# Performance work log

Measured on AMD Instinct MI355X. Metric: run time of the kernel, lower is better.

## Reference

```python
import jax, jax.numpy as jnp
import numpy as np

N, E, F_IN, F_HID, F_OUT = 100000, 1600000, 128, 128, 64


def setup_inputs() -> dict:
    key = jax.random.key(0)
    k = jax.random.split(key, 6)
    x = jax.random.normal(k[0], (N, F_IN), dtype=jnp.float32)
    edge_index = jax.random.randint(k[1], (2, E), 0, N, dtype=jnp.int32)
    # Glorot-ish init for the two GCNConv linear layers (+ bias, PyG default bias=True)
    W1 = jax.random.normal(k[2], (F_IN, F_HID), dtype=jnp.float32) * (1.0 / np.sqrt(F_IN))
    b1 = jnp.zeros((F_HID,), dtype=jnp.float32)
    W2 = jax.random.normal(k[3], (F_HID, F_OUT), dtype=jnp.float32) * (1.0 / np.sqrt(F_HID))
    b2 = jnp.zeros((F_OUT,), dtype=jnp.float32)
    return {"x": x, "edge_index": edge_index, "W1": W1, "b1": b1, "W2": W2, "b2": b2}


def reference(x, edge_index, W1, b1, W2, b2):
    n = x.shape[0]
    row, col = edge_index[0], edge_index[1]
    # gcn_norm with add_self_loops=True, edge_weight=None -> all-ones weights
    loop = jnp.arange(n, dtype=row.dtype)
    row = jnp.concatenate([row, loop])
    col = jnp.concatenate([col, loop])
    w = jnp.ones(row.shape[0], dtype=x.dtype)
    deg = jax.ops.segment_sum(w, col, num_segments=n)  # in-degree at targets
    dis = jnp.where(deg > 0, jax.lax.rsqrt(jnp.maximum(deg, 1.0)), 0.0)
    norm = dis[row] * w * dis[col]  # [E+N]

    def gcn_conv(h, W, b):
        h = h @ W                       # linear transform first (PyG order)
        msg = h[row] * norm[:, None]    # gather + scale, [E+N, d]
        return jax.ops.segment_sum(msg, col, num_segments=n) + b  # scatter-add

    h = jax.nn.relu(gcn_conv(x, W1, b1))
    # dropout is identity in eval mode
    return gcn_conv(h, W2, b2)
```

## Files before the change

kernel.cpp:

```cpp
#include <hip/hip_runtime.h>

#define F1 128
#define F2 64
#define BSH 9
#define BSZ 512
#define BFILL_CAP 12288

typedef unsigned int u32;
typedef unsigned short u16;
typedef __attribute__((ext_vector_type(8))) short bf16x8;
typedef __attribute__((ext_vector_type(4))) float f32x4;

__device__ __forceinline__ u32 bf16rne(float f) {
    u32 u = __float_as_uint(f);
    return (u + 0x7FFFu + ((u >> 16) & 1u)) >> 16;
}
__device__ __forceinline__ u32 pack2(float lo, float hi) {
    return bf16rne(lo) | (bf16rne(hi) << 16);
}
__device__ __forceinline__ float bflo(u32 u) { return __uint_as_float(u << 16); }
__device__ __forceinline__ float bfhi(u32 u) { return __uint_as_float(u & 0xFFFF0000u); }

__device__ __forceinline__ void acc8(float* ax, uint4 v) {
    ax[0] += bflo(v.x); ax[1] += bfhi(v.x);
    ax[2] += bflo(v.y); ax[3] += bfhi(v.y);
    ax[4] += bflo(v.z); ax[5] += bfhi(v.z);
    ax[6] += bflo(v.w); ax[7] += bfhi(v.w);
}


__global__ __launch_bounds__(256) void k_bhist(const int* __restrict__ colv,
                                               int* __restrict__ bucket_cnt, int E) {
    __shared__ int l[256];
    int t = threadIdx.x;
    l[t] = 0;
    __syncthreads();
    for (int e = blockIdx.x * blockDim.x + t; e < E; e += gridDim.x * blockDim.x)
        atomicAdd(&l[colv[e] >> BSH], 1);
    __syncthreads();
    if (l[t]) atomicAdd(&bucket_cnt[t], l[t]);
}

__global__ __launch_bounds__(256) void k_bscan(const int* __restrict__ bucket_cnt,
                                               int* __restrict__ bucket_base,
                                               int* __restrict__ bucket_cur,
                                               int* __restrict__ rowptr_last,
                                               int NB, int E) {
    __shared__ int s[256];
    int t = threadIdx.x;
    int v = (t < NB) ? bucket_cnt[t] : 0;
    s[t] = v;
    __syncthreads();
    for (int d = 1; d < 256; d <<= 1) {
        int u = (t >= d) ? s[t - d] : 0;
        __syncthreads();
        s[t] += u;
        __syncthreads();
    }
    int excl = s[t] - v;
    if (t < NB) { bucket_base[t] = excl; bucket_cur[t] = excl; }
    if (t == NB - 1) bucket_base[NB] = s[t];
    if (t == 0) *rowptr_last = E;
}

__global__ __launch_bounds__(256) void k_part(const int* __restrict__ rowv,
                                              const int* __restrict__ colv,
                                              int* __restrict__ bucket_cur,
                                              u32* __restrict__ ebuf, int E) {
    __shared__ int lcnt[256], lexcl[256], lcur[256], lbase[256];
    __shared__ int stot;
    __shared__ u32 sval[4096];
    __shared__ u16 sbkt[4096];
    int t = threadIdx.x;
    lcnt[t] = 0;
    __syncthreads();
    int rows[16], cols[16];
    int e0 = blockIdx.x * 4096;
#pragma unroll
    for (int it = 0; it < 16; it++) {
        int e = e0 + it * 256 + t;
        bool v = e < E;
        cols[it] = v ? colv[e] : -1;
        rows[it] = v ? rowv[e] : 0;
        if (v) atomicAdd(&lcnt[cols[it] >> BSH], 1);
    }
    __syncthreads();
    int v = lcnt[t];
    int s = v;
    lexcl[t] = s;
    __syncthreads();
    for (int d = 1; d < 256; d <<= 1) {
        int u = (t >= d) ? lexcl[t - d] : 0;
        __syncthreads();
        lexcl[t] += u;
        __syncthreads();
    }
    int incl = lexcl[t];
    __syncthreads();
    lexcl[t] = incl - v;
    lcur[t] = incl - v;
    if (v) lbase[t] = atomicAdd(&bucket_cur[t], v);
    if (t == 255) stot = incl;
    __syncthreads();
#pragma unroll
    for (int it = 0; it < 16; it++) {
        if (cols[it] >= 0) {
            int b = cols[it] >> BSH;
            int pos = atomicAdd(&lcur[b], 1);
            sval[pos] = ((u32)(cols[it] & (BSZ - 1)) << 17) | (u32)rows[it];
            sbkt[pos] = (u16)b;
        }
    }
    __syncthreads();
    int total = stot;
    for (int i = t; i < total; i += 256) {
        int b = sbkt[i];
        ebuf[lbase[b] + (i - lexcl[b])] = sval[i];
    }
}

__global__ __launch_bounds__(512) void k_bfill(const u32* __restrict__ ebuf,
                                               const int* __restrict__ bucket_base,
                                               int* __restrict__ rowptr,
                                               float* __restrict__ dis,
                                               int* __restrict__ adj, int N) {
    __shared__ int cnt[BSZ], scn[BSZ], cur[BSZ];
    __shared__ int sadj[BFILL_CAP];
    int t = threadIdx.x;
    int b = blockIdx.x;
    int e0 = bucket_base[b], e1 = bucket_base[b + 1];
    int len = e1 - e0;
    cnt[t] = 0;
    __syncthreads();
    for (int i = e0 + t; i < e1; i += BSZ)
        atomicAdd(&cnt[ebuf[i] >> 17], 1);
    __syncthreads();
    scn[t] = cnt[t];
    __syncthreads();
    for (int d = 1; d < BSZ; d <<= 1) {
        int u = (t >= d) ? scn[t - d] : 0;
        __syncthreads();
        scn[t] += u;
        __syncthreads();
    }
    int excl = scn[t] - cnt[t];
    cur[t] = excl;
    int node = (b << BSH) + t;
    if (node < N) {
        rowptr[node] = e0 + excl;
        dis[node] = rsqrtf((float)(cnt[t] + 1));
    }
    __syncthreads();
    if (len <= BFILL_CAP) {
        for (int i = e0 + t; i < e1; i += BSZ) {
            u32 p = ebuf[i];
            int c = p >> 17;
            int r = (int)(p & 0x1FFFFu);
            int pos = atomicAdd(&cur[c], 1);
            sadj[pos] = r;
        }
        __syncthreads();
        for (int i = t; i < len; i += BSZ)
            adj[e0 + i] = sadj[i];
    } else {
        for (int i = e0 + t; i < e1; i += BSZ) {
            u32 p = ebuf[i];
            int c = p >> 17;
            int r = (int)(p & 0x1FFFFu);
            int pos = atomicAdd(&cur[c], 1);
            adj[e0 + pos] = r;
        }
    }
}


__device__ __forceinline__ void wprep_do(const float* __restrict__ W,
                                         uint4* __restrict__ wf, int NBc, int t) {
    int lane = t & 63;
    int rem = t >> 6;
    int nb = rem % NBc;
    int kb = rem / NBc;
    int C = NBc * 16;
    int col = nb * 16 + (lane & 15);
    int krow = kb * 32 + (lane >> 4) * 8;
    u32 w[4];
#pragma unroll
    for (int p = 0; p < 4; p++) {
        float lo = W[(size_t)(krow + 2 * p) * C + col];
        float hi = W[(size_t)(krow + 2 * p + 1) * C + col];
        w[p] = pack2(lo, hi);
    }
    wf[t] = make_uint4(w[0], w[1], w[2], w[3]);
}

__global__ __launch_bounds__(256) void k_wprep(const float* __restrict__ W1,
                                               const float* __restrict__ W2,
                                               uint4* __restrict__ w1f,
                                               uint4* __restrict__ w2f) {
    int blk = blockIdx.x;
    if (blk < 8) wprep_do(W1, w1f, 8, blk * 256 + threadIdx.x);
    else         wprep_do(W2, w2f, 4, (blk - 8) * 256 + threadIdx.x);
}


__global__ __launch_bounds__(256, 4) void k_gemm1(const float* __restrict__ x,
                                                  const uint4* __restrict__ w1f,
                                                  const float* __restrict__ dis,
                                                  u16* __restrict__ gb, int N) {
    int lane = threadIdx.x & 63;
    int wave = threadIdx.x >> 6;
    int m = lane & 15, quad = lane >> 4;
    int row0 = blockIdx.x * 64 + wave * 16;
    int arow = min(row0 + m, N - 1);
    const float* xr = x + (size_t)arow * F1 + quad * 8;
    bf16x8 a[4];
#pragma unroll
    for (int kb = 0; kb < 4; kb++) {
        float4 lo = *(const float4*)(xr + kb * 32);
        float4 hi = *(const float4*)(xr + kb * 32 + 4);
        a[kb][0] = (short)bf16rne(lo.x); a[kb][1] = (short)bf16rne(lo.y);
        a[kb][2] = (short)bf16rne(lo.z); a[kb][3] = (short)bf16rne(lo.w);
        a[kb][4] = (short)bf16rne(hi.x); a[kb][5] = (short)bf16rne(hi.y);
        a[kb][6] = (short)bf16rne(hi.z); a[kb][7] = (short)bf16rne(hi.w);
    }
    f32x4 acc[8];
#pragma unroll
    for (int nb = 0; nb < 8; nb++) acc[nb] = (f32x4)(0.0f);
#pragma unroll
    for (int nb = 0; nb < 8; nb++) {
#pragma unroll
        for (int kb = 0; kb < 4; kb++) {
            uint4 braw = w1f[(kb * 8 + nb) * 64 + lane];
            bf16x8 bf = *(bf16x8*)&braw;
            acc[nb] = __builtin_amdgcn_mfma_f32_16x16x32_bf16(a[kb], bf, acc[nb], 0, 0, 0);
        }
    }
    float dv[4];
    int rbase = row0 + quad * 4;
#pragma unroll
    for (int reg = 0; reg < 4; reg++) dv[reg] = dis[min(rbase + reg, N - 1)];
#pragma unroll
    for (int reg = 0; reg < 4; reg++) {
        int r = rbase + reg;
        if (r < N) {
            u16* gr = gb + (size_t)r * F1 + m;
#pragma unroll
            for (int nb = 0; nb < 8; nb++)
                gr[nb * 16] = (u16)bf16rne(acc[nb][reg] * dv[reg]);
        }
    }
}


__global__ __launch_bounds__(256) void k_agg1(const uint4* __restrict__ g1,
                                              const int* __restrict__ rowptr,
                                              const int* __restrict__ adj,
                                              const float* __restrict__ dis,
                                              const float* __restrict__ b,
                                              uint4* __restrict__ z, int N) {
    int node = __builtin_amdgcn_readfirstlane(blockIdx.x * 4 + (threadIdx.x >> 6));
    if (node >= N) return;
    int lane = threadIdx.x & 63;
    int grp = lane >> 4;
    int sub = lane & 15;
    float ax[8];
#pragma unroll
    for (int i = 0; i < 8; i++) ax[i] = 0.0f;
    int s = rowptr[node], e = rowptr[node + 1];
    if (grp == 0) acc8(ax, g1[(size_t)node * 16 + sub]);
    const uint4 z4 = make_uint4(0u, 0u, 0u, 0u);
    int i0 = s + grp;
    bool p0 = i0 < e, p1 = i0 + 4 < e, p2 = i0 + 8 < e, p3 = i0 + 12 < e;
    int c0 = 0, c1 = 0, c2 = 0, c3 = 0;
    if (p0) c0 = adj[i0];
    if (p1) c1 = adj[i0 + 4];
    if (p2) c2 = adj[i0 + 8];
    if (p3) c3 = adj[i0 + 12];
    for (int j = s; j < e; j += 16) {
        uint4 v0 = z4, v1 = z4, v2 = z4, v3 = z4;
        if (p0) v0 = g1[(size_t)c0 * 16 + sub];
        if (p1) v1 = g1[(size_t)c1 * 16 + sub];
        if (p2) v2 = g1[(size_t)c2 * 16 + sub];
        if (p3) v3 = g1[(size_t)c3 * 16 + sub];
        int in0 = j + 16 + grp;
        p0 = in0 < e; p1 = in0 + 4 < e; p2 = in0 + 8 < e; p3 = in0 + 12 < e;
        if (p0) c0 = adj[in0];
        if (p1) c1 = adj[in0 + 4];
        if (p2) c2 = adj[in0 + 8];
        if (p3) c3 = adj[in0 + 12];
        acc8(ax, v0);
        acc8(ax, v1);
        acc8(ax, v2);
        acc8(ax, v3);
    }
#pragma unroll
    for (int i = 0; i < 8; i++) {
        ax[i] += __shfl_xor(ax[i], 16);
        ax[i] += __shfl_xor(ax[i], 32);
    }
    if (grp == 0) {
        float d = dis[node];
        float4 b0 = *(const float4*)(b + 8 * sub);
        float4 b1 = *(const float4*)(b + 8 * sub + 4);
        float o[8];
        o[0] = fmaxf(fmaf(d, ax[0], b0.x), 0.0f);
        o[1] = fmaxf(fmaf(d, ax[1], b0.y), 0.0f);
        o[2] = fmaxf(fmaf(d, ax[2], b0.z), 0.0f);
        o[3] = fmaxf(fmaf(d, ax[3], b0.w), 0.0f);
        o[4] = fmaxf(fmaf(d, ax[4], b1.x), 0.0f);
        o[5] = fmaxf(fmaf(d, ax[5], b1.y), 0.0f);
        o[6] = fmaxf(fmaf(d, ax[6], b1.z), 0.0f);
        o[7] = fmaxf(fmaf(d, ax[7], b1.w), 0.0f);
        uint4 ov;
        ov.x = pack2(o[0], o[1]); ov.y = pack2(o[2], o[3]);
        ov.z = pack2(o[4], o[5]); ov.w = pack2(o[6], o[7]);
        z[(size_t)node * 16 + sub] = ov;
    }
}


__global__ __launch_bounds__(256, 4) void k_gemm2(const u32* __restrict__ z,
                                                  const uint4* __restrict__ w2f,
                                                  const float* __restrict__ dis,
                                                  u16* __restrict__ gb, int N) {
    int lane = threadIdx.x & 63;
    int wave = threadIdx.x >> 6;
    int m = lane & 15, quad = lane >> 4;
    int row0 = blockIdx.x * 64 + wave * 16;
    int arow = min(row0 + m, N - 1);
    const u32* zr = z + (size_t)arow * 64 + quad * 4;
    bf16x8 a[4];
#pragma unroll
    for (int kb = 0; kb < 4; kb++) {
        uint4 za = *(const uint4*)(zr + kb * 16);
        a[kb] = *(bf16x8*)&za;
    }
    f32x4 acc[4];
#pragma unroll
    for (int nb = 0; nb < 4; nb++) acc[nb] = (f32x4)(0.0f);
#pragma unroll
    for (int nb = 0; nb < 4; nb++) {
#pragma unroll
        for (int kb = 0; kb < 4; kb++) {
            uint4 braw = w2f[(kb * 4 + nb) * 64 + lane];
            bf16x8 bf = *(bf16x8*)&braw;
            acc[nb] = __builtin_amdgcn_mfma_f32_16x16x32_bf16(a[kb], bf, acc[nb], 0, 0, 0);
        }
    }
    float dv[4];
    int rbase = row0 + quad * 4;
#pragma unroll
    for (int reg = 0; reg < 4; reg++) dv[reg] = dis[min(rbase + reg, N - 1)];
#pragma unroll
    for (int reg = 0; reg < 4; reg++) {
        int r = rbase + reg;
        if (r < N) {
            u16* gr = gb + (size_t)r * F2 + m;
#pragma unroll
            for (int nb = 0; nb < 4; nb++)
                gr[nb * 16] = (u16)bf16rne(acc[nb][reg] * dv[reg]);
        }
    }
}


__global__ __launch_bounds__(256) void k_agg2(const uint4* __restrict__ g,
                                              const int* __restrict__ rowptr,
                                              const int* __restrict__ adj,
                                              const float* __restrict__ dis,
                                              const float* __restrict__ b,
                                              float* __restrict__ out, int N) {
    int node = __builtin_amdgcn_readfirstlane(blockIdx.x * 4 + (threadIdx.x >> 6));
    if (node >= N) return;
    int lane = threadIdx.x & 63;
    int grp = lane >> 3;
    int sub = lane & 7;
    float ax[8];
#pragma unroll
    for (int i = 0; i < 8; i++) ax[i] = 0.0f;
    int s = rowptr[node], e = rowptr[node + 1];
    if (grp == 0) acc8(ax, g[(size_t)node * 8 + sub]);
    const uint4 z4 = make_uint4(0u, 0u, 0u, 0u);
    int i0 = s + grp;
    bool p0 = i0 < e, p1 = i0 + 8 < e, p2 = i0 + 16 < e, p3 = i0 + 24 < e;
    int c0 = 0, c1 = 0, c2 = 0, c3 = 0;
    if (p0) c0 = adj[i0];
    if (p1) c1 = adj[i0 + 8];
    if (p2) c2 = adj[i0 + 16];
    if (p3) c3 = adj[i0 + 24];
    for (int j = s; j < e; j += 32) {
        uint4 v0 = z4, v1 = z4, v2 = z4, v3 = z4;
        if (p0) v0 = g[(size_t)c0 * 8 + sub];
        if (p1) v1 = g[(size_t)c1 * 8 + sub];
        if (p2) v2 = g[(size_t)c2 * 8 + sub];
        if (p3) v3 = g[(size_t)c3 * 8 + sub];
        int in0 = j + 32 + grp;
        p0 = in0 < e; p1 = in0 + 8 < e; p2 = in0 + 16 < e; p3 = in0 + 24 < e;
        if (p0) c0 = adj[in0];
        if (p1) c1 = adj[in0 + 8];
        if (p2) c2 = adj[in0 + 16];
        if (p3) c3 = adj[in0 + 24];
        acc8(ax, v0);
        acc8(ax, v1);
        acc8(ax, v2);
        acc8(ax, v3);
    }
#pragma unroll
    for (int i = 0; i < 8; i++) {
        ax[i] += __shfl_xor(ax[i], 8);
        ax[i] += __shfl_xor(ax[i], 16);
        ax[i] += __shfl_xor(ax[i], 32);
    }
    if (grp == 0) {
        float d = dis[node];
        float4 b0 = *(const float4*)(b + 8 * sub);
        float4 b1 = *(const float4*)(b + 8 * sub + 4);
        float4 o0, o1;
        o0.x = fmaf(d, ax[0], b0.x); o0.y = fmaf(d, ax[1], b0.y);
        o0.z = fmaf(d, ax[2], b0.z); o0.w = fmaf(d, ax[3], b0.w);
        o1.x = fmaf(d, ax[4], b1.x); o1.y = fmaf(d, ax[5], b1.y);
        o1.z = fmaf(d, ax[6], b1.z); o1.w = fmaf(d, ax[7], b1.w);
        float4* op = (float4*)(out + (size_t)node * F2 + 8 * sub);
        op[0] = o0;
        op[1] = o1;
    }
}


extern "C" void kernel_launch(void* const* d_in, const int* in_sizes, int n_in,
                              void* d_out, int out_size, void* d_ws, size_t ws_size,
                              hipStream_t stream) {
    const float* x  = (const float*)d_in[0];
    const int*   ei = (const int*)d_in[1];
    const float* W1 = (const float*)d_in[2];
    const float* b1 = (const float*)d_in[3];
    const float* W2 = (const float*)d_in[4];
    const float* b2 = (const float*)d_in[5];
    float* out = (float*)d_out;

    const int N = in_sizes[0] / F1;
    const int E = in_sizes[1] / 2;
    const int NB = (N + BSZ - 1) >> BSH;
    const int* rowv = ei;
    const int* colv = ei + E;

    char* ws = (char*)d_ws;
    size_t off = 0;
    auto take = [&](size_t bytes) -> void* {
        void* p = ws + off;
        off += (bytes + 255) & ~(size_t)255;
        return p;
    };
    u16*   g1b     = (u16*)take((size_t)N * F1 * 2);
    u32*   zb      = (u32*)take((size_t)N * 64 * 4);
    u16*   g2b     = g1b;
    u32*   ebuf    = (u32*)g1b;
    float* dis     = (float*)take((size_t)N * 4);
    int*   rowptr  = (int*)take((size_t)(N + 1) * 4);
    int*   adj     = (int*)take((size_t)E * 4);
    uint4* w1f     = (uint4*)take(4 * 8 * 64 * 16);
    uint4* w2f     = (uint4*)take(4 * 4 * 64 * 16);
    int*   bucket_cnt  = (int*)take(256 * 4);
    int*   bucket_base = (int*)take(257 * 4);
    int*   bucket_cur  = (int*)take(256 * 4);

    hipMemsetAsync(bucket_cnt, 0, 256 * 4, stream);

    k_wprep<<<12, 256, 0, stream>>>(W1, W2, w1f, w2f);

    k_bhist<<<256, 256, 0, stream>>>(colv, bucket_cnt, E);
    k_bscan<<<1, 256, 0, stream>>>(bucket_cnt, bucket_base, bucket_cur, rowptr + N, NB, E);
    k_part<<<(E + 4095) / 4096, 256, 0, stream>>>(rowv, colv, bucket_cur, ebuf, E);
    k_bfill<<<NB, BSZ, 0, stream>>>(ebuf, bucket_base, rowptr, dis, adj, N);

    int gblocks = (N + 63) / 64;
    k_gemm1<<<gblocks, 256, 0, stream>>>(x, w1f, dis, g1b, N);
    k_agg1<<<(N + 3) / 4, 256, 0, stream>>>((const uint4*)g1b, rowptr, adj, dis, b1,
                                            (uint4*)zb, N);
    k_gemm2<<<gblocks, 256, 0, stream>>>(zb, w2f, dis, g2b, N);
    k_agg2<<<(N + 3) / 4, 256, 0, stream>>>((const uint4*)g2b, rowptr, adj, dis, b2, out, N);
}
```

Measured before the change: 274.4 us.

## Fuse second GEMM into first aggregation and drop bucket scan kernel

The layer-2 linear transform now runs inside the layer-1 aggregation kernel. Each wave shuffles its node's post-ReLU bf16 row into an MFMA A operand and writes the scaled 64-wide result directly. This removes the z intermediate buffer's write and read and one kernel launch, but wastes most MFMA rows and adds register pressure to the aggregation. The standalone bucket scan kernel is also removed: its prefix sum is recomputed redundantly in the partition and fill kernels.

```diff
diff --git a/kernel.cpp b/kernel.cpp
--- a/kernel.cpp
+++ b/kernel.cpp
@@ -41,33 +41,12 @@
     if (l[t]) atomicAdd(&bucket_cnt[t], l[t]);
 }
 
-__global__ __launch_bounds__(256) void k_bscan(const int* __restrict__ bucket_cnt,
-                                               int* __restrict__ bucket_base,
-                                               int* __restrict__ bucket_cur,
-                                               int* __restrict__ rowptr_last,
-                                               int NB, int E) {
-    __shared__ int s[256];
-    int t = threadIdx.x;
-    int v = (t < NB) ? bucket_cnt[t] : 0;
-    s[t] = v;
-    __syncthreads();
-    for (int d = 1; d < 256; d <<= 1) {
-        int u = (t >= d) ? s[t - d] : 0;
-        __syncthreads();
-        s[t] += u;
-        __syncthreads();
-    }
-    int excl = s[t] - v;
-    if (t < NB) { bucket_base[t] = excl; bucket_cur[t] = excl; }
-    if (t == NB - 1) bucket_base[NB] = s[t];
-    if (t == 0) *rowptr_last = E;
-}
-
 __global__ __launch_bounds__(256) void k_part(const int* __restrict__ rowv,
                                               const int* __restrict__ colv,
+                                              const int* __restrict__ bucket_cnt,
                                               int* __restrict__ bucket_cur,
                                               u32* __restrict__ ebuf, int E) {
-    __shared__ int lcnt[256], lexcl[256], lcur[256], lbase[256];
+    __shared__ int lcnt[256], lexcl[256], lcur[256], lbase[256], gscan[256];
     __shared__ int stot;
     __shared__ u32 sval[4096];
     __shared__ u16 sbkt[4096];
@@ -84,22 +63,26 @@
         rows[it] = v ? rowv[e] : 0;
         if (v) atomicAdd(&lcnt[cols[it] >> BSH], 1);
     }
+    int bc = bucket_cnt[t];
     __syncthreads();
     int v = lcnt[t];
-    int s = v;
-    lexcl[t] = s;
+    lexcl[t] = v;
+    gscan[t] = bc;
     __syncthreads();
     for (int d = 1; d < 256; d <<= 1) {
-        int u = (t >= d) ? lexcl[t - d] : 0;
-        __syncthreads();
-        lexcl[t] += u;
+        int u1 = (t >= d) ? lexcl[t - d] : 0;
+        int u2 = (t >= d) ? gscan[t - d] : 0;
+        __syncthreads();
+        lexcl[t] += u1;
+        gscan[t] += u2;
         __syncthreads();
     }
     int incl = lexcl[t];
+    int gincl = gscan[t];
     __syncthreads();
     lexcl[t] = incl - v;
     lcur[t] = incl - v;
-    if (v) lbase[t] = atomicAdd(&bucket_cur[t], v);
+    if (v) lbase[t] = (gincl - bc) + atomicAdd(&bucket_cur[t], v);
     if (t == 255) stot = incl;
     __syncthreads();
 #pragma unroll
@@ -120,18 +103,28 @@
 }
 
 __global__ __launch_bounds__(512) void k_bfill(const u32* __restrict__ ebuf,
-                                               const int* __restrict__ bucket_base,
+                                               const int* __restrict__ bucket_cnt,
                                                int* __restrict__ rowptr,
                                                float* __restrict__ dis,
-                                               int* __restrict__ adj, int N) {
+                                               int* __restrict__ adj, int N, int E) {
     __shared__ int cnt[BSZ], scn[BSZ], cur[BSZ];
+    __shared__ int bb[256];
     __shared__ int sadj[BFILL_CAP];
     int t = threadIdx.x;
     int b = blockIdx.x;
-    int e0 = bucket_base[b], e1 = bucket_base[b + 1];
+    if (t < 256) bb[t] = bucket_cnt[t];
+    cnt[t] = 0;
+    __syncthreads();
+    for (int d = 1; d < 256; d <<= 1) {
+        int u = (t >= d && t < 256) ? bb[t - d] : 0;
+        __syncthreads();
+        if (t < 256) bb[t] += u;
+        __syncthreads();
+    }
+    int e1 = bb[b];
+    int e0 = e1 - bucket_cnt[b];
     int len = e1 - e0;
-    cnt[t] = 0;
-    __syncthreads();
+    if (b == 0 && t == 0) rowptr[N] = E;
     for (int i = e0 + t; i < e1; i += BSZ)
         atomicAdd(&cnt[ebuf[i] >> 17], 1);
     __syncthreads();
@@ -257,7 +250,8 @@
                                               const int* __restrict__ adj,
                                               const float* __restrict__ dis,
                                               const float* __restrict__ b,
-                                              uint4* __restrict__ z, int N) {
+                                              const uint4* __restrict__ w2f,
+                                              u16* __restrict__ g2, int N) {
     int node = __builtin_amdgcn_readfirstlane(blockIdx.x * 4 + (threadIdx.x >> 6));
     if (node >= N) return;
     int lane = threadIdx.x & 63;
@@ -298,68 +292,45 @@
         ax[i] += __shfl_xor(ax[i], 16);
         ax[i] += __shfl_xor(ax[i], 32);
     }
-    if (grp == 0) {
-        float d = dis[node];
-        float4 b0 = *(const float4*)(b + 8 * sub);
-        float4 b1 = *(const float4*)(b + 8 * sub + 4);
-        float o[8];
-        o[0] = fmaxf(fmaf(d, ax[0], b0.x), 0.0f);
-        o[1] = fmaxf(fmaf(d, ax[1], b0.y), 0.0f);
-        o[2] = fmaxf(fmaf(d, ax[2], b0.z), 0.0f);
-        o[3] = fmaxf(fmaf(d, ax[3], b0.w), 0.0f);
-        o[4] = fmaxf(fmaf(d, ax[4], b1.x), 0.0f);
-        o[5] = fmaxf(fmaf(d, ax[5], b1.y), 0.0f);
-        o[6] = fmaxf(fmaf(d, ax[6], b1.z), 0.0f);
-        o[7] = fmaxf(fmaf(d, ax[7], b1.w), 0.0f);
-        uint4 ov;
-        ov.x = pack2(o[0], o[1]); ov.y = pack2(o[2], o[3]);
-        ov.z = pack2(o[4], o[5]); ov.w = pack2(o[6], o[7]);
-        z[(size_t)node * 16 + sub] = ov;
-    }
-}
-
-
-__global__ __launch_bounds__(256, 4) void k_gemm2(const u32* __restrict__ z,
-                                                  const uint4* __restrict__ w2f,
-                                                  const float* __restrict__ dis,
-                                                  u16* __restrict__ gb, int N) {
-    int lane = threadIdx.x & 63;
-    int wave = threadIdx.x >> 6;
-    int m = lane & 15, quad = lane >> 4;
-    int row0 = blockIdx.x * 64 + wave * 16;
-    int arow = min(row0 + m, N - 1);
-    const u32* zr = z + (size_t)arow * 64 + quad * 4;
-    bf16x8 a[4];
+    float d = dis[node];
+    float4 b0 = *(const float4*)(b + 8 * sub);
+    float4 b1 = *(const float4*)(b + 8 * sub + 4);
+    float o[8];
+    o[0] = fmaxf(fmaf(d, ax[0], b0.x), 0.0f);
+    o[1] = fmaxf(fmaf(d, ax[1], b0.y), 0.0f);
+    o[2] = fmaxf(fmaf(d, ax[2], b0.z), 0.0f);
+    o[3] = fmaxf(fmaf(d, ax[3], b0.w), 0.0f);
+    o[4] = fmaxf(fmaf(d, ax[4], b1.x), 0.0f);
+    o[5] = fmaxf(fmaf(d, ax[5], b1.y), 0.0f);
+    o[6] = fmaxf(fmaf(d, ax[6], b1.z), 0.0f);
+    o[7] = fmaxf(fmaf(d, ax[7], b1.w), 0.0f);
+    u32 opk[4];
+    opk[0] = pack2(o[0], o[1]);
+    opk[1] = pack2(o[2], o[3]);
+    opk[2] = pack2(o[4], o[5]);
+    opk[3] = pack2(o[6], o[7]);
+    bf16x8 af[4];
 #pragma unroll
     for (int kb = 0; kb < 4; kb++) {
-        uint4 za = *(const uint4*)(zr + kb * 16);
-        a[kb] = *(bf16x8*)&za;
-    }
-    f32x4 acc[4];
-#pragma unroll
-    for (int nb = 0; nb < 4; nb++) acc[nb] = (f32x4)(0.0f);
+        int src = 4 * kb + grp;
+        uint4 tmp;
+        tmp.x = (u32)__shfl((int)opk[0], src);
+        tmp.y = (u32)__shfl((int)opk[1], src);
+        tmp.z = (u32)__shfl((int)opk[2], src);
+        tmp.w = (u32)__shfl((int)opk[3], src);
+        af[kb] = *(bf16x8*)&tmp;
+    }
+    u16* gr = g2 + (size_t)node * F2;
 #pragma unroll
     for (int nb = 0; nb < 4; nb++) {
+        f32x4 acc = (f32x4)(0.0f);
 #pragma unroll
         for (int kb = 0; kb < 4; kb++) {
             uint4 braw = w2f[(kb * 4 + nb) * 64 + lane];
             bf16x8 bf = *(bf16x8*)&braw;
-            acc[nb] = __builtin_amdgcn_mfma_f32_16x16x32_bf16(a[kb], bf, acc[nb], 0, 0, 0);
-        }
-    }
-    float dv[4];
-    int rbase = row0 + quad * 4;
-#pragma unroll
-    for (int reg = 0; reg < 4; reg++) dv[reg] = dis[min(rbase + reg, N - 1)];
-#pragma unroll
-    for (int reg = 0; reg < 4; reg++) {
-        int r = rbase + reg;
-        if (r < N) {
-            u16* gr = gb + (size_t)r * F2 + m;
-#pragma unroll
-            for (int nb = 0; nb < 4; nb++)
-                gr[nb * 16] = (u16)bf16rne(acc[nb][reg] * dv[reg]);
-        }
+            acc = __builtin_amdgcn_mfma_f32_16x16x32_bf16(af[kb], bf, acc, 0, 0, 0);
+        }
+        if (grp == 0) gr[nb * 16 + sub] = (u16)bf16rne(acc[0] * d);
     }
 }
 
@@ -452,31 +423,27 @@
         return p;
     };
     u16*   g1b     = (u16*)take((size_t)N * F1 * 2);
-    u32*   zb      = (u32*)take((size_t)N * 64 * 4);
-    u16*   g2b     = g1b;
+    u16*   g2b     = (u16*)take((size_t)N * F2 * 2);
     u32*   ebuf    = (u32*)g1b;
     float* dis     = (float*)take((size_t)N * 4);
     int*   rowptr  = (int*)take((size_t)(N + 1) * 4);
     int*   adj     = (int*)take((size_t)E * 4);
     uint4* w1f     = (uint4*)take(4 * 8 * 64 * 16);
     uint4* w2f     = (uint4*)take(4 * 4 * 64 * 16);
-    int*   bucket_cnt  = (int*)take(256 * 4);
-    int*   bucket_base = (int*)take(257 * 4);
-    int*   bucket_cur  = (int*)take(256 * 4);
-
-    hipMemsetAsync(bucket_cnt, 0, 256 * 4, stream);
+    int*   bucket_cnt  = (int*)take(512 * 4);
+    int*   bucket_cur  = bucket_cnt + 256;
+
+    hipMemsetAsync(bucket_cnt, 0, 512 * 4, stream);
 
     k_wprep<<<12, 256, 0, stream>>>(W1, W2, w1f, w2f);
 
     k_bhist<<<256, 256, 0, stream>>>(colv, bucket_cnt, E);
-    k_bscan<<<1, 256, 0, stream>>>(bucket_cnt, bucket_base, bucket_cur, rowptr + N, NB, E);
-    k_part<<<(E + 4095) / 4096, 256, 0, stream>>>(rowv, colv, bucket_cur, ebuf, E);
-    k_bfill<<<NB, BSZ, 0, stream>>>(ebuf, bucket_base, rowptr, dis, adj, N);
+    k_part<<<(E + 4095) / 4096, 256, 0, stream>>>(rowv, colv, bucket_cnt, bucket_cur, ebuf, E);
+    k_bfill<<<NB, BSZ, 0, stream>>>(ebuf, bucket_cnt, rowptr, dis, adj, N, E);
 
     int gblocks = (N + 63) / 64;
     k_gemm1<<<gblocks, 256, 0, stream>>>(x, w1f, dis, g1b, N);
     k_agg1<<<(N + 3) / 4, 256, 0, stream>>>((const uint4*)g1b, rowptr, adj, dis, b1,
-                                            (uint4*)zb, N);
-    k_gemm2<<<gblocks, 256, 0, stream>>>(zb, w2f, dis, g2b, N);
+                                            w2f, g2b, N);
     k_agg2<<<(N + 3) / 4, 256, 0, stream>>>((const uint4*)g2b, rowptr, adj, dis, b2, out, N);
 }
```

After: 286.9 us. 4.6% more time.

## Fuse CSR build stages with weight prep and GEMM1 to cut launches

Applied to the files above, without the earlier changes.

Fuses the bucket histogram with a per-node degree count and the weight repacking into one kernel. A second kernel runs edge partitioning and GEMM1 as disjoint block ranges, so the partition can overlap the matmul. The separate scan kernel is removed: the bucket offsets are recomputed inside the partition and fill kernels. GEMM1 now takes its normalisation from atomic degree counts instead of waiting for the CSR fill. The partition stage is halved, the edge buffer moves to the z buffer, and the agg2 unroll drops from 4 to 2. The cost is extra global atomics on deg, an extra memset, and redundant scans in every block.

```diff
diff --git a/kernel.cpp b/kernel.cpp
--- a/kernel.cpp
+++ b/kernel.cpp
@@ -5,6 +5,7 @@
 #define BSH 9
 #define BSZ 512
 #define BFILL_CAP 12288
+#define PSTAGE 2048
 
 typedef unsigned int u32;
 typedef unsigned short u16;
@@ -26,151 +27,6 @@
     ax[2] += bflo(v.y); ax[3] += bfhi(v.y);
     ax[4] += bflo(v.z); ax[5] += bfhi(v.z);
     ax[6] += bflo(v.w); ax[7] += bfhi(v.w);
-}
-
-
-__global__ __launch_bounds__(256) void k_bhist(const int* __restrict__ colv,
-                                               int* __restrict__ bucket_cnt, int E) {
-    __shared__ int l[256];
-    int t = threadIdx.x;
-    l[t] = 0;
-    __syncthreads();
-    for (int e = blockIdx.x * blockDim.x + t; e < E; e += gridDim.x * blockDim.x)
-        atomicAdd(&l[colv[e] >> BSH], 1);
-    __syncthreads();
-    if (l[t]) atomicAdd(&bucket_cnt[t], l[t]);
-}
-
-__global__ __launch_bounds__(256) void k_bscan(const int* __restrict__ bucket_cnt,
-                                               int* __restrict__ bucket_base,
-                                               int* __restrict__ bucket_cur,
-                                               int* __restrict__ rowptr_last,
-                                               int NB, int E) {
-    __shared__ int s[256];
-    int t = threadIdx.x;
-    int v = (t < NB) ? bucket_cnt[t] : 0;
-    s[t] = v;
-    __syncthreads();
-    for (int d = 1; d < 256; d <<= 1) {
-        int u = (t >= d) ? s[t - d] : 0;
-        __syncthreads();
-        s[t] += u;
-        __syncthreads();
-    }
-    int excl = s[t] - v;
-    if (t < NB) { bucket_base[t] = excl; bucket_cur[t] = excl; }
-    if (t == NB - 1) bucket_base[NB] = s[t];
-    if (t == 0) *rowptr_last = E;
-}
-
-__global__ __launch_bounds__(256) void k_part(const int* __restrict__ rowv,
-                                              const int* __restrict__ colv,
-                                              int* __restrict__ bucket_cur,
-                                              u32* __restrict__ ebuf, int E) {
-    __shared__ int lcnt[256], lexcl[256], lcur[256], lbase[256];
-    __shared__ int stot;
-    __shared__ u32 sval[4096];
-    __shared__ u16 sbkt[4096];
-    int t = threadIdx.x;
-    lcnt[t] = 0;
-    __syncthreads();
-    int rows[16], cols[16];
-    int e0 = blockIdx.x * 4096;
-#pragma unroll
-    for (int it = 0; it < 16; it++) {
-        int e = e0 + it * 256 + t;
-        bool v = e < E;
-        cols[it] = v ? colv[e] : -1;
-        rows[it] = v ? rowv[e] : 0;
-        if (v) atomicAdd(&lcnt[cols[it] >> BSH], 1);
-    }
-    __syncthreads();
-    int v = lcnt[t];
-    int s = v;
-    lexcl[t] = s;
-    __syncthreads();
-    for (int d = 1; d < 256; d <<= 1) {
-        int u = (t >= d) ? lexcl[t - d] : 0;
-        __syncthreads();
-        lexcl[t] += u;
-        __syncthreads();
-    }
-    int incl = lexcl[t];
-    __syncthreads();
-    lexcl[t] = incl - v;
-    lcur[t] = incl - v;
-    if (v) lbase[t] = atomicAdd(&bucket_cur[t], v);
-    if (t == 255) stot = incl;
-    __syncthreads();
-#pragma unroll
-    for (int it = 0; it < 16; it++) {
-        if (cols[it] >= 0) {
-            int b = cols[it] >> BSH;
-            int pos = atomicAdd(&lcur[b], 1);
-            sval[pos] = ((u32)(cols[it] & (BSZ - 1)) << 17) | (u32)rows[it];
-            sbkt[pos] = (u16)b;
-        }
-    }
-    __syncthreads();
-    int total = stot;
-    for (int i = t; i < total; i += 256) {
-        int b = sbkt[i];
-        ebuf[lbase[b] + (i - lexcl[b])] = sval[i];
-    }
-}
-
-__global__ __launch_bounds__(512) void k_bfill(const u32* __restrict__ ebuf,
-                                               const int* __restrict__ bucket_base,
-                                               int* __restrict__ rowptr,
-                                               float* __restrict__ dis,
-                                               int* __restrict__ adj, int N) {
-    __shared__ int cnt[BSZ], scn[BSZ], cur[BSZ];
-    __shared__ int sadj[BFILL_CAP];
-    int t = threadIdx.x;
-    int b = blockIdx.x;
-    int e0 = bucket_base[b], e1 = bucket_base[b + 1];
-    int len = e1 - e0;
-    cnt[t] = 0;
-    __syncthreads();
-    for (int i = e0 + t; i < e1; i += BSZ)
-        atomicAdd(&cnt[ebuf[i] >> 17], 1);
-    __syncthreads();
-    scn[t] = cnt[t];
-    __syncthreads();
-    for (int d = 1; d < BSZ; d <<= 1) {
-        int u = (t >= d) ? scn[t - d] : 0;
-        __syncthreads();
-        scn[t] += u;
-        __syncthreads();
-    }
-    int excl = scn[t] - cnt[t];
-    cur[t] = excl;
-    int node = (b << BSH) + t;
-    if (node < N) {
-        rowptr[node] = e0 + excl;
-        dis[node] = rsqrtf((float)(cnt[t] + 1));
-    }
-    __syncthreads();
-    if (len <= BFILL_CAP) {
-        for (int i = e0 + t; i < e1; i += BSZ) {
-            u32 p = ebuf[i];
-            int c = p >> 17;
-            int r = (int)(p & 0x1FFFFu);
-            int pos = atomicAdd(&cur[c], 1);
-            sadj[pos] = r;
-        }
-        __syncthreads();
-        for (int i = t; i < len; i += BSZ)
-            adj[e0 + i] = sadj[i];
-    } else {
-        for (int i = e0 + t; i < e1; i += BSZ) {
-            u32 p = ebuf[i];
-            int c = p >> 17;
-            int r = (int)(p & 0x1FFFFu);
-            int pos = atomicAdd(&cur[c], 1);
-            adj[e0 + pos] = r;
-        }
-    }
 }
 
 
@@ -193,60 +49,206 @@
     wf[t] = make_uint4(w[0], w[1], w[2], w[3]);
 }
 
-__global__ __launch_bounds__(256) void k_wprep(const float* __restrict__ W1,
-                                               const float* __restrict__ W2,
-                                               uint4* __restrict__ w1f,
-                                               uint4* __restrict__ w2f) {
+
+__global__ __launch_bounds__(256) void k_bw(const int* __restrict__ colv,
+                                            int* __restrict__ bucket_cnt,
+                                            int* __restrict__ deg,
+                                            const float* __restrict__ W1,
+                                            const float* __restrict__ W2,
+                                            uint4* __restrict__ w1f,
+                                            uint4* __restrict__ w2f, int E) {
+    __shared__ int l[256];
     int blk = blockIdx.x;
-    if (blk < 8) wprep_do(W1, w1f, 8, blk * 256 + threadIdx.x);
-    else         wprep_do(W2, w2f, 4, (blk - 8) * 256 + threadIdx.x);
-}
-
-
-__global__ __launch_bounds__(256, 4) void k_gemm1(const float* __restrict__ x,
-                                                  const uint4* __restrict__ w1f,
-                                                  const float* __restrict__ dis,
-                                                  u16* __restrict__ gb, int N) {
-    int lane = threadIdx.x & 63;
-    int wave = threadIdx.x >> 6;
-    int m = lane & 15, quad = lane >> 4;
-    int row0 = blockIdx.x * 64 + wave * 16;
-    int arow = min(row0 + m, N - 1);
-    const float* xr = x + (size_t)arow * F1 + quad * 8;
-    bf16x8 a[4];
-#pragma unroll
-    for (int kb = 0; kb < 4; kb++) {
-        float4 lo = *(const float4*)(xr + kb * 32);
-        float4 hi = *(const float4*)(xr + kb * 32 + 4);
-        a[kb][0] = (short)bf16rne(lo.x); a[kb][1] = (short)bf16rne(lo.y);
-        a[kb][2] = (short)bf16rne(lo.z); a[kb][3] = (short)bf16rne(lo.w);
-        a[kb][4] = (short)bf16rne(hi.x); a[kb][5] = (short)bf16rne(hi.y);
-        a[kb][6] = (short)bf16rne(hi.z); a[kb][7] = (short)bf16rne(hi.w);
-    }
-    f32x4 acc[8];
-#pragma unroll
-    for (int nb = 0; nb < 8; nb++) acc[nb] = (f32x4)(0.0f);
-#pragma unroll
-    for (int nb = 0; nb < 8; nb++) {
+    int t = threadIdx.x;
+    if (blk < 256) {
+        l[t] = 0;
+        __syncthreads();
+        for (int e = blk * 256 + t; e < E; e += 256 * 256) {
+            int c = colv[e];
+            atomicAdd(&l[c >> BSH], 1);
+            atomicAdd(&deg[c], 1);
+        }
+        __syncthreads();
+        if (l[t]) atomicAdd(&bucket_cnt[t], l[t]);
+    } else {
+        int b2 = blk - 256;
+        if (b2 < 8) wprep_do(W1, w1f, 8, b2 * 256 + t);
+        else        wprep_do(W2, w2f, 4, (b2 - 8) * 256 + t);
+    }
+}
+
+
+__global__ __launch_bounds__(256, 4) void k_pg(const int* __restrict__ rowv,
+                                               const int* __restrict__ colv,
+                                               const int* __restrict__ bucket_cnt,
+                                               int* __restrict__ bucket_cur,
+                                               u32* __restrict__ ebuf, int E, int PB,
+                                               const float* __restrict__ x,
+                                               const uint4* __restrict__ w1f,
+                                               const int* __restrict__ deg,
+                                               u16* __restrict__ gb, int N) {
+    if ((int)blockIdx.x < PB) {
+        __shared__ int lcnt[256], lexcl[256], lcur[256], lbase[256], gscan[256];
+        __shared__ int stot;
+        __shared__ u32 sval[PSTAGE];
+        __shared__ u16 sbkt[PSTAGE];
+        int t = threadIdx.x;
+        lcnt[t] = 0;
+        __syncthreads();
+        int rows[8], cols[8];
+        int e0 = blockIdx.x * PSTAGE;
+#pragma unroll
+        for (int it = 0; it < 8; it++) {
+            int e = e0 + it * 256 + t;
+            bool v = e < E;
+            cols[it] = v ? colv[e] : -1;
+            rows[it] = v ? rowv[e] : 0;
+            if (v) atomicAdd(&lcnt[cols[it] >> BSH], 1);
+        }
+        int bc = bucket_cnt[t];
+        __syncthreads();
+        int v = lcnt[t];
+        lexcl[t] = v;
+        gscan[t] = bc;
+        __syncthreads();
+        for (int d = 1; d < 256; d <<= 1) {
+            int u1 = (t >= d) ? lexcl[t - d] : 0;
+            int u2 = (t >= d) ? gscan[t - d] : 0;
+            __syncthreads();
+            lexcl[t] += u1;
+            gscan[t] += u2;
+            __syncthreads();
+        }
+        int incl = lexcl[t];
+        int gincl = gscan[t];
+        __syncthreads();
+        lexcl[t] = incl - v;
+        lcur[t] = incl - v;
+        if (v) lbase[t] = (gincl - bc) + atomicAdd(&bucket_cur[t], v);
+        if (t == 255) stot = incl;
+        __syncthreads();
+#pragma unroll
+        for (int it = 0; it < 8; it++) {
+            if (cols[it] >= 0) {
+                int b = cols[it] >> BSH;
+                int pos = atomicAdd(&lcur[b], 1);
+                sval[pos] = ((u32)(cols[it] & (BSZ - 1)) << 17) | (u32)rows[it];
+                sbkt[pos] = (u16)b;
+            }
+        }
+        __syncthreads();
+        int total = stot;
+        for (int i = t; i < total; i += 256) {
+            int b = sbkt[i];
+            ebuf[lbase[b] + (i - lexcl[b])] = sval[i];
+        }
+    } else {
+        int bid = (int)blockIdx.x - PB;
+        int lane = threadIdx.x & 63;
+        int wave = threadIdx.x >> 6;
+        int m = lane & 15, quad = lane >> 4;
+        int row0 = bid * 64 + wave * 16;
+        int arow = min(row0 + m, N - 1);
+        const float* xr = x + (size_t)arow * F1 + quad * 8;
+        bf16x8 a[4];
 #pragma unroll
         for (int kb = 0; kb < 4; kb++) {
-            uint4 braw = w1f[(kb * 8 + nb) * 64 + lane];
-            bf16x8 bf = *(bf16x8*)&braw;
-            acc[nb] = __builtin_amdgcn_mfma_f32_16x16x32_bf16(a[kb], bf, acc[nb], 0, 0, 0);
-        }
-    }
-    float dv[4];
-    int rbase = row0 + quad * 4;
-#pragma unroll
-    for (int reg = 0; reg < 4; reg++) dv[reg] = dis[min(rbase + reg, N - 1)];
-#pragma unroll
-    for (int reg = 0; reg < 4; reg++) {
-        int r = rbase + reg;
-        if (r < N) {
-            u16* gr = gb + (size_t)r * F1 + m;
-#pragma unroll
-            for (int nb = 0; nb < 8; nb++)
-                gr[nb * 16] = (u16)bf16rne(acc[nb][reg] * dv[reg]);
+            float4 lo = *(const float4*)(xr + kb * 32);
+            float4 hi = *(const float4*)(xr + kb * 32 + 4);
+            a[kb][0] = (short)bf16rne(lo.x); a[kb][1] = (short)bf16rne(lo.y);
+            a[kb][2] = (short)bf16rne(lo.z); a[kb][3] = (short)bf16rne(lo.w);
+            a[kb][4] = (short)bf16rne(hi.x); a[kb][5] = (short)bf16rne(hi.y);
+            a[kb][6] = (short)bf16rne(hi.z); a[kb][7] = (short)bf16rne(hi.w);
+        }
+        f32x4 acc[8];
+#pragma unroll
+        for (int nb = 0; nb < 8; nb++) acc[nb] = (f32x4)(0.0f);
+#pragma unroll
+        for (int nb = 0; nb < 8; nb++) {
+#pragma unroll
+            for (int kb = 0; kb < 4; kb++) {
+                uint4 braw = w1f[(kb * 8 + nb) * 64 + lane];
+                bf16x8 bf = *(bf16x8*)&braw;
+                acc[nb] = __builtin_amdgcn_mfma_f32_16x16x32_bf16(a[kb], bf, acc[nb], 0, 0, 0);
+            }
+        }
+        float dv[4];
+        int rbase = row0 + quad * 4;
+#pragma unroll
+        for (int reg = 0; reg < 4; reg++)
+            dv[reg] = rsqrtf((float)deg[min(rbase + reg, N - 1)] + 1.0f);
+#pragma unroll
+        for (int reg = 0; reg < 4; reg++) {
+            int r = rbase + reg;
+            if (r < N) {
+                u16* gr = gb + (size_t)r * F1 + m;
+#pragma unroll
+                for (int nb = 0; nb < 8; nb++)
+                    gr[nb * 16] = (u16)bf16rne(acc[nb][reg] * dv[reg]);
+            }
+        }
+    }
+}
+
+
+__global__ __launch_bounds__(512) void k_bfill(const u32* __restrict__ ebuf,
+                                               const int* __restrict__ bucket_cnt,
+                                               int* __restrict__ rowptr,
+                                               float* __restrict__ dis,
+                                               int* __restrict__ adj, int N, int E) {
+    __shared__ int cnt[BSZ], scn[BSZ], cur[BSZ];
+    __shared__ int bb[256];
+    __shared__ int sadj[BFILL_CAP];
+    int t = threadIdx.x;
+    int b = blockIdx.x;
+    if (t < 256) bb[t] = bucket_cnt[t];
+    cnt[t] = 0;
+    __syncthreads();
+    for (int d = 1; d < 256; d <<= 1) {
+        int u = (t >= d && t < 256) ? bb[t - d] : 0;
+        __syncthreads();
+        if (t < 256) bb[t] += u;
+        __syncthreads();
+    }
+    int e1 = bb[b];
+    int e0 = e1 - bucket_cnt[b];
+    int len = e1 - e0;
+    if (b == 0 && t == 0) rowptr[N] = E;
+    for (int i = e0 + t; i < e1; i += BSZ)
+        atomicAdd(&cnt[ebuf[i] >> 17], 1);
+    __syncthreads();
+    scn[t] = cnt[t];
+    __syncthreads();
+    for (int d = 1; d < BSZ; d <<= 1) {
+        int u = (t >= d) ? scn[t - d] : 0;
+        __syncthreads();
+        scn[t] += u;
+        __syncthreads();
+    }
+    int excl = scn[t] - cnt[t];
+    cur[t] = excl;
+    int node = (b << BSH) + t;
+    if (node < N) {
+        rowptr[node] = e0 + excl;
+        dis[node] = rsqrtf((float)(cnt[t] + 1));
+    }
+    __syncthreads();
+    if (len <= BFILL_CAP) {
+        for (int i = e0 + t; i < e1; i += BSZ) {
+            u32 p = ebuf[i];
+            int c = p >> 17;
+            int pos = atomicAdd(&cur[c], 1);
+            sadj[pos] = (int)(p & 0x1FFFFu);
+        }
+        __syncthreads();
+        for (int i = t; i < len; i += BSZ)
+            adj[e0 + i] = sadj[i];
+    } else {
+        for (int i = e0 + t; i < e1; i += BSZ) {
+            u32 p = ebuf[i];
+            int c = p >> 17;
+            int pos = atomicAdd(&cur[c], 1);
+            adj[e0 + pos] = (int)(p & 0x1FFFFu);
         }
     }
 }
@@ -382,28 +384,20 @@
     if (grp == 0) acc8(ax, g[(size_t)node * 8 + sub]);
     const uint4 z4 = make_uint4(0u, 0u, 0u, 0u);
     int i0 = s + grp;
-    bool p0 = i0 < e, p1 = i0 + 8 < e, p2 = i0 + 16 < e, p3 = i0 + 24 < e;
-    int c0 = 0, c1 = 0, c2 = 0, c3 = 0;
+    bool p0 = i0 < e, p1 = i0 + 8 < e;
+    int c0 = 0, c1 = 0;
     if (p0) c0 = adj[i0];
     if (p1) c1 = adj[i0 + 8];
-    if (p2) c2 = adj[i0 + 16];
-    if (p3) c3 = adj[i0 + 24];
-    for (int j = s; j < e; j += 32) {
-        uint4 v0 = z4, v1 = z4, v2 = z4, v3 = z4;
+    for (int j = s; j < e; j += 16) {
+        uint4 v0 = z4, v1 = z4;
         if (p0) v0 = g[(size_t)c0 * 8 + sub];
         if (p1) v1 = g[(size_t)c1 * 8 + sub];
-        if (p2) v2 = g[(size_t)c2 * 8 + sub];
-        if (p3) v3 = g[(size_t)c3 * 8 + sub];
-        int in0 = j + 32 + grp;
-        p0 = in0 < e; p1 = in0 + 8 < e; p2 = in0 + 16 < e; p3 = in0 + 24 < e;
+        int in0 = j + 16 + grp;
+        p0 = in0 < e; p1 = in0 + 8 < e;
         if (p0) c0 = adj[in0];
         if (p1) c1 = adj[in0 + 8];
-        if (p2) c2 = adj[in0 + 16];
-        if (p3) c3 = adj[in0 + 24];
         acc8(ax, v0);
         acc8(ax, v1);
-        acc8(ax, v2);
-        acc8(ax, v3);
     }
 #pragma unroll
     for (int i = 0; i < 8; i++) {
@@ -454,27 +448,28 @@
     u16*   g1b     = (u16*)take((size_t)N * F1 * 2);
     u32*   zb      = (u32*)take((size_t)N * 64 * 4);
     u16*   g2b     = g1b;
-    u32*   ebuf    = (u32*)g1b;
+    u32*   ebuf    = zb;
     float* dis     = (float*)take((size_t)N * 4);
+    int*   deg     = (int*)take((size_t)N * 4);
     int*   rowptr  = (int*)take((size_t)(N + 1) * 4);
     int*   adj     = (int*)take((size_t)E * 4);
     uint4* w1f     = (uint4*)take(4 * 8 * 64 * 16);
     uint4* w2f     = (uint4*)take(4 * 4 * 64 * 16);
-    int*   bucket_cnt  = (int*)take(256 * 4);
-    int*   bucket_base = (int*)take(257 * 4);
-    int*   bucket_cur  = (int*)take(256 * 4);
-
-    hipMemsetAsync(bucket_cnt, 0, 256 * 4, stream);
-
-    k_wprep<<<12, 256, 0, stream>>>(W1, W2, w1f, w2f);
-
-    k_bhist<<<256, 256, 0, stream>>>(colv, bucket_cnt, E);
-    k_bscan<<<1, 256, 0, stream>>>(bucket_cnt, bucket_base, bucket_cur, rowptr + N, NB, E);
-    k_part<<<(E + 4095) / 4096, 256, 0, stream>>>(rowv, colv, bucket_cur, ebuf, E);
-    k_bfill<<<NB, BSZ, 0, stream>>>(ebuf, bucket_base, rowptr, dis, adj, N);
-
+    int*   bucket_cnt  = (int*)take(512 * 4);
+    int*   bucket_cur  = bucket_cnt + 256;
+
+    hipMemsetAsync(bucket_cnt, 0, 512 * 4, stream);
+    hipMemsetAsync(deg, 0, (size_t)N * 4, stream);
+
+    k_bw<<<268, 256, 0, stream>>>(colv, bucket_cnt, deg, W1, W2, w1f, w2f, E);
+
+    int PB = (E + PSTAGE - 1) / PSTAGE;
     int gblocks = (N + 63) / 64;
-    k_gemm1<<<gblocks, 256, 0, stream>>>(x, w1f, dis, g1b, N);
+    k_pg<<<PB + gblocks, 256, 0, stream>>>(rowv, colv, bucket_cnt, bucket_cur, ebuf,
+                                           E, PB, x, w1f, deg, g1b, N);
+
+    k_bfill<<<NB, BSZ, 0, stream>>>(ebuf, bucket_cnt, rowptr, dis, adj, N, E);
+
     k_agg1<<<(N + 3) / 4, 256, 0, stream>>>((const uint4*)g1b, rowptr, adj, dis, b1,
                                             (uint4*)zb, N);
     k_gemm2<<<gblocks, 256, 0, stream>>>(zb, w2f, dis, g2b, N);
```

Result: slower. 330.0 us (+20.3%).
